# Optimization experiments

Hardware: AMD Instinct MI355X
Metric: run time of the kernel (lower is better)

The kernel has to match this reference:

```python
import jax, jax.numpy as jnp
import numpy as np

B, IN_DIM, UNITS = 16384, 3072, 3072  # batch, input_dim=3*unit1, units=3*unit2


def setup_inputs() -> dict:
    key = jax.random.key(0)
    k1, k2, k3 = jax.random.split(key, 3)
    inputs = jax.random.normal(k1, (B, IN_DIM), dtype=jnp.float32)
    # original init: uniform [0, 0.01) for w, zeros for b (gpe_bias = [0, 0])
    w = jax.random.uniform(k2, (IN_DIM, UNITS), dtype=jnp.float32, minval=0.0, maxval=0.01)
    b = jnp.zeros((UNITS,), dtype=jnp.float32)
    # per-unit binary diagonal mask, stored as [units, input_dim]
    mask = jax.random.randint(k3, (UNITS, IN_DIM), 0, 2, dtype=jnp.int32)
    return {"inputs": inputs, "w": w, "b": b, "mask": mask}


def reference(inputs, w, b, mask):
    # Original: p = transpose(s @ inputs^T, [2,0,1]) -> [batch, units, input_dim]
    #           f = diag_part(p @ w) + b            -> [batch, units]
    # Since s[u] = diag(mask[u]), this is exactly:
    #   f[b,u] = sum_i inputs[b,i] * mask[u,i] * w[i,u] + b[u]
    # i.e. a single masked GEMM with effective weight w * mask^T.
    w_eff = w * mask.T.astype(w.dtype)  # [input_dim, units]
    return inputs @ w_eff + b
```

## Files before the change

### kernel.cpp

```cpp
#include <hip/hip_runtime.h>

#define BATCH 16384
#define KDIM  3072
#define NDIM  3072

typedef __bf16 bf16;
typedef bf16  bf16x8  __attribute__((ext_vector_type(8)));
typedef float f32x16  __attribute__((ext_vector_type(16)));

__device__ __forceinline__ void g2l16(const bf16* g, bf16* l) {
    __builtin_amdgcn_global_load_lds(
        (__attribute__((address_space(1))) unsigned int*)g,
        (__attribute__((address_space(3))) unsigned int*)l,
        16, 0, 0);
}

__global__ __launch_bounds__(256) void cvt_a_kernel(const float* __restrict__ in,
                                                    bf16* __restrict__ out) {
    const long idx = (long)blockIdx.x * 256 + threadIdx.x;
    const float4* in4 = (const float4*)in;
    float4 a = in4[idx * 2];
    float4 b = in4[idx * 2 + 1];
    bf16x8 o;
    o[0] = (bf16)a.x; o[1] = (bf16)a.y; o[2] = (bf16)a.z; o[3] = (bf16)a.w;
    o[4] = (bf16)b.x; o[5] = (bf16)b.y; o[6] = (bf16)b.z; o[7] = (bf16)b.w;
    ((bf16x8*)out)[idx] = o;
}

__global__ __launch_bounds__(256) void weff_kernel(const float* __restrict__ w,
                                                   const int* __restrict__ mask,
                                                   bf16* __restrict__ wt) {
    __shared__ float tile[32][33];
    const int i0 = blockIdx.x * 32;
    const int u0 = blockIdx.y * 32;
    const int tx = threadIdx.x, ty = threadIdx.y;
#pragma unroll
    for (int r = 0; r < 4; r++)
        tile[ty + 8 * r][tx] = w[(long)(i0 + ty + 8 * r) * NDIM + u0 + tx];
    __syncthreads();
#pragma unroll
    for (int r = 0; r < 4; r++) {
        int u = u0 + ty + 8 * r;
        int i = i0 + tx;
        float v = tile[tx][ty + 8 * r] * (float)mask[(long)u * KDIM + i];
        wt[(long)u * KDIM + i] = (bf16)v;
    }
}


#define STAGE_UNIT(Q, KT, KS) do {                                              \
    const long ko_ = (long)(KT) * 64 + ((KS) >> 1) * 32;                        \
    const bf16* gs_ = (((KS) & 1) == 0) ? gA : gB;                              \
    bf16* ds_ = &lds[(Q) * 32768 + ((((KS) & 1) == 0) ? 0 : 16384)              \
                     + ((KS) >> 1) * 8192 + tid * 8];                           \
    g2l16(gs_ + ko_, ds_);                                                      \
    g2l16(gs_ + ko_ + (long)128 * KDIM, ds_ + 4096);                            \
} while (0)

#define PHASE(KS, P, DOSTAGE, KT, VM) do {                                      \
    asm volatile("" ::: "memory");       \
    const bf16* bp_ = &lds[(P) * 32768];                                        \
    const int cOff_ = ((KS) >> 1) * 8192 + (((((KS) & 1) * 2) + kb) ^ sx3) * 8; \
    bf16x8 a0_ = *(const bf16x8*)(bp_ + aOff0 + cOff_);                         \
    bf16x8 a1_ = *(const bf16x8*)(bp_ + aOff1 + cOff_);                         \
    bf16x8 a2_ = *(const bf16x8*)(bp_ + aOff2 + cOff_);                         \
    bf16x8 a3_ = *(const bf16x8*)(bp_ + aOff3 + cOff_);                         \
    bf16x8 b0_ = *(const bf16x8*)(bp_ + bOff0 + cOff_);                         \
    bf16x8 b1_ = *(const bf16x8*)(bp_ + bOff1 + cOff_);                         \
    if (DOSTAGE) { STAGE_UNIT((P) ^ 1, KT, KS); }                               \
    asm volatile("" ::: "memory");          \
    __builtin_amdgcn_s_barrier();                                               \
    asm volatile("s_waitcnt lgkmcnt(0)" ::: "memory");                          \
    __builtin_amdgcn_sched_barrier(0);   \
    __builtin_amdgcn_s_setprio(1);                                              \
    acc[0][0] = __builtin_amdgcn_mfma_f32_32x32x16_bf16(a0_, b0_, acc[0][0], 0, 0, 0); \
    acc[0][1] = __builtin_amdgcn_mfma_f32_32x32x16_bf16(a0_, b1_, acc[0][1], 0, 0, 0); \
    acc[1][0] = __builtin_amdgcn_mfma_f32_32x32x16_bf16(a1_, b0_, acc[1][0], 0, 0, 0); \
    acc[1][1] = __builtin_amdgcn_mfma_f32_32x32x16_bf16(a1_, b1_, acc[1][1], 0, 0, 0); \
    acc[2][0] = __builtin_amdgcn_mfma_f32_32x32x16_bf16(a2_, b0_, acc[2][0], 0, 0, 0); \
    acc[2][1] = __builtin_amdgcn_mfma_f32_32x32x16_bf16(a2_, b1_, acc[2][1], 0, 0, 0); \
    acc[3][0] = __builtin_amdgcn_mfma_f32_32x32x16_bf16(a3_, b0_, acc[3][0], 0, 0, 0); \
    acc[3][1] = __builtin_amdgcn_mfma_f32_32x32x16_bf16(a3_, b1_, acc[3][1], 0, 0, 0); \
    __builtin_amdgcn_s_setprio(0);                                              \
    if ((VM) >= 0)                                                              \
        asm volatile("s_waitcnt vmcnt(%0)" :: "n"((VM) < 0 ? 0 : (VM)) : "memory"); \
    __builtin_amdgcn_s_barrier();                                               \
} while (0)

__global__ __launch_bounds__(512, 2) void gemm_kernel(const bf16* __restrict__ A,
                                                      const bf16* __restrict__ Bt,
                                                      const float* __restrict__ bias,
                                                      float* __restrict__ C) {
    __shared__ __align__(16) bf16 lds[2 * 32768];

    const int tid  = threadIdx.x;
    const int lane = tid & 63;
    const int wv   = tid >> 6;
    const int rl   = lane & 31;
    const int kb   = lane >> 5;
    const int sx3  = rl & 3;

    const int lid = blockIdx.y * gridDim.x + blockIdx.x;
    const int sid = (lid & 7) * 96 + (lid >> 3);
    const long m0 = (long)(sid / 12) * 256;
    const long n0 = (long)(sid % 12) * 256;

    const int waveM = (wv >> 2) * 128;
    const int waveN = (wv & 3) * 64;

    const int srow = tid >> 2;
    const int sc   = (tid & 3) ^ (srow & 3);
    const bf16* gA = A  + (m0 + srow) * KDIM + sc * 8;
    const bf16* gB = Bt + (n0 + srow) * KDIM + sc * 8;

    const int aOff0 = (waveM + 0 * 32 + rl) * 32;
    const int aOff1 = (waveM + 1 * 32 + rl) * 32;
    const int aOff2 = (waveM + 2 * 32 + rl) * 32;
    const int aOff3 = (waveM + 3 * 32 + rl) * 32;
    const int bOff0 = 16384 + (waveN + 0 * 32 + rl) * 32;
    const int bOff1 = 16384 + (waveN + 1 * 32 + rl) * 32;

    f32x16 acc[4][2] = {};

    STAGE_UNIT(0, 0, 0);
    STAGE_UNIT(0, 0, 1);
    STAGE_UNIT(0, 0, 2);
    STAGE_UNIT(0, 0, 3);
    asm volatile("s_waitcnt vmcnt(4)" ::: "memory");
    __builtin_amdgcn_s_barrier();

    const int NT = KDIM / 64;
#pragma unroll 2
    for (int t = 0; t < NT - 1; ++t) {
        const int p = t & 1;
        PHASE(0, p, 1, t + 1, -1);
        PHASE(1, p, 1, t + 1, 4);
        PHASE(2, p, 1, t + 1, -1);
        PHASE(3, p, 1, t + 1, 4);
    }
    PHASE(0, 1, 0, 0, -1);
    PHASE(1, 1, 0, 0, 0);
    PHASE(2, 1, 0, 0, -1);
    PHASE(3, 1, 0, 0, -1);

#pragma unroll
    for (int ni = 0; ni < 2; ++ni) {
        const long col = n0 + waveN + ni * 32 + rl;
        const float bv = bias[col];
#pragma unroll
        for (int mi = 0; mi < 4; ++mi) {
            const long rbase = m0 + waveM + mi * 32 + 4 * kb;
#pragma unroll
            for (int g = 0; g < 4; ++g)
#pragma unroll
                for (int t = 0; t < 4; ++t)
                    C[(rbase + 8 * g + t) * NDIM + col] = acc[mi][ni][4 * g + t] + bv;
        }
    }
}

__global__ __launch_bounds__(256) void naive_kernel(const float* __restrict__ x,
                                                    const float* __restrict__ w,
                                                    const float* __restrict__ bias,
                                                    const int* __restrict__ mask,
                                                    float* __restrict__ out) {
    const long idx = (long)blockIdx.x * 256 + threadIdx.x;
    const long bi = idx / NDIM;
    const int u = (int)(idx % NDIM);
    float s = 0.f;
    for (int k = 0; k < KDIM; k++)
        s += x[bi * KDIM + k] * w[(long)k * NDIM + u] * (float)mask[(long)u * KDIM + k];
    out[idx] = s + bias[u];
}

extern "C" void kernel_launch(void* const* d_in, const int* in_sizes, int n_in,
                              void* d_out, int out_size, void* d_ws, size_t ws_size,
                              hipStream_t stream) {
    const float* x    = (const float*)d_in[0];
    const float* w    = (const float*)d_in[1];
    const float* bias = (const float*)d_in[2];
    const int*   mask = (const int*)d_in[3];
    float* out = (float*)d_out;

    const size_t needA = (size_t)BATCH * KDIM * sizeof(bf16);
    const size_t needW = (size_t)NDIM * KDIM * sizeof(bf16);

    if (ws_size < needA + needW) {
        const long total = (long)BATCH * NDIM;
        naive_kernel<<<(int)(total / 256), 256, 0, stream>>>(x, w, bias, mask, out);
        return;
    }

    bf16* Abf = (bf16*)d_ws;
    bf16* Wt  = (bf16*)((char*)d_ws + needA);

    cvt_a_kernel<<<(BATCH * (KDIM / 8)) / 256, 256, 0, stream>>>(x, Abf);
    weff_kernel<<<dim3(KDIM / 32, NDIM / 32), dim3(32, 8), 0, stream>>>(w, mask, Wt);
    gemm_kernel<<<dim3(NDIM / 256, BATCH / 256), 512, 0, stream>>>(Abf, Wt, bias, out);
}
```

Before: 684.4 us.

## Restructure GEMM main loop with 16x16x32 MFMA, quadrant phases and register fragment reuse

The bf16 GEMM main loop now uses 16x16x32 MFMA instead of 32x32x16. Each wave's output is split into four quadrants computed in separate phases, with A and B fragments held in registers and reused across phases. LDS staging is reorganised into half-tile units with an 8-way XOR swizzle over 64-wide K rows, and loads for later K tiles are interleaved across the phases. The aim is fewer LDS reads per MFMA and better overlap of global-to-LDS transfers with compute, at the cost of more register pressure and a wrap-around prefetch at the loop tail.

```diff
diff --git a/kernel.cpp b/kernel.cpp
--- a/kernel.cpp
+++ b/kernel.cpp
@@ -6,7 +6,7 @@
 
 typedef __bf16 bf16;
 typedef bf16  bf16x8  __attribute__((ext_vector_type(8)));
-typedef float f32x16  __attribute__((ext_vector_type(16)));
+typedef float f32x4   __attribute__((ext_vector_type(4)));
 
 __device__ __forceinline__ void g2l16(const bf16* g, bf16* l) {
     __builtin_amdgcn_global_load_lds(
@@ -47,46 +47,6 @@
     }
 }
 
-
-#define STAGE_UNIT(Q, KT, KS) do {                                              \
-    const long ko_ = (long)(KT) * 64 + ((KS) >> 1) * 32;                        \
-    const bf16* gs_ = (((KS) & 1) == 0) ? gA : gB;                              \
-    bf16* ds_ = &lds[(Q) * 32768 + ((((KS) & 1) == 0) ? 0 : 16384)              \
-                     + ((KS) >> 1) * 8192 + tid * 8];                           \
-    g2l16(gs_ + ko_, ds_);                                                      \
-    g2l16(gs_ + ko_ + (long)128 * KDIM, ds_ + 4096);                            \
-} while (0)
-
-#define PHASE(KS, P, DOSTAGE, KT, VM) do {                                      \
-    asm volatile("" ::: "memory");       \
-    const bf16* bp_ = &lds[(P) * 32768];                                        \
-    const int cOff_ = ((KS) >> 1) * 8192 + (((((KS) & 1) * 2) + kb) ^ sx3) * 8; \
-    bf16x8 a0_ = *(const bf16x8*)(bp_ + aOff0 + cOff_);                         \
-    bf16x8 a1_ = *(const bf16x8*)(bp_ + aOff1 + cOff_);                         \
-    bf16x8 a2_ = *(const bf16x8*)(bp_ + aOff2 + cOff_);                         \
-    bf16x8 a3_ = *(const bf16x8*)(bp_ + aOff3 + cOff_);                         \
-    bf16x8 b0_ = *(const bf16x8*)(bp_ + bOff0 + cOff_);                         \
-    bf16x8 b1_ = *(const bf16x8*)(bp_ + bOff1 + cOff_);                         \
-    if (DOSTAGE) { STAGE_UNIT((P) ^ 1, KT, KS); }                               \
-    asm volatile("" ::: "memory");          \
-    __builtin_amdgcn_s_barrier();                                               \
-    asm volatile("s_waitcnt lgkmcnt(0)" ::: "memory");                          \
-    __builtin_amdgcn_sched_barrier(0);   \
-    __builtin_amdgcn_s_setprio(1);                                              \
-    acc[0][0] = __builtin_amdgcn_mfma_f32_32x32x16_bf16(a0_, b0_, acc[0][0], 0, 0, 0); \
-    acc[0][1] = __builtin_amdgcn_mfma_f32_32x32x16_bf16(a0_, b1_, acc[0][1], 0, 0, 0); \
-    acc[1][0] = __builtin_amdgcn_mfma_f32_32x32x16_bf16(a1_, b0_, acc[1][0], 0, 0, 0); \
-    acc[1][1] = __builtin_amdgcn_mfma_f32_32x32x16_bf16(a1_, b1_, acc[1][1], 0, 0, 0); \
-    acc[2][0] = __builtin_amdgcn_mfma_f32_32x32x16_bf16(a2_, b0_, acc[2][0], 0, 0, 0); \
-    acc[2][1] = __builtin_amdgcn_mfma_f32_32x32x16_bf16(a2_, b1_, acc[2][1], 0, 0, 0); \
-    acc[3][0] = __builtin_amdgcn_mfma_f32_32x32x16_bf16(a3_, b0_, acc[3][0], 0, 0, 0); \
-    acc[3][1] = __builtin_amdgcn_mfma_f32_32x32x16_bf16(a3_, b1_, acc[3][1], 0, 0, 0); \
-    __builtin_amdgcn_s_setprio(0);                                              \
-    if ((VM) >= 0)                                                              \
-        asm volatile("s_waitcnt vmcnt(%0)" :: "n"((VM) < 0 ? 0 : (VM)) : "memory"); \
-    __builtin_amdgcn_s_barrier();                                               \
-} while (0)
-
 __global__ __launch_bounds__(512, 2) void gemm_kernel(const bf16* __restrict__ A,
                                                       const bf16* __restrict__ Bt,
                                                       const float* __restrict__ bias,
@@ -96,67 +56,135 @@
     const int tid  = threadIdx.x;
     const int lane = tid & 63;
     const int wv   = tid >> 6;
-    const int rl   = lane & 31;
-    const int kb   = lane >> 5;
-    const int sx3  = rl & 3;
+    const int l15  = lane & 15;
+    const int l4   = lane >> 4;
+    const int sx   = l15 & 7;
+    const int wm   = (wv >> 2) * 64;
+    const int wn   = (wv & 3) * 32;
 
     const int lid = blockIdx.y * gridDim.x + blockIdx.x;
     const int sid = (lid & 7) * 96 + (lid >> 3);
     const long m0 = (long)(sid / 12) * 256;
     const long n0 = (long)(sid % 12) * 256;
 
-    const int waveM = (wv >> 2) * 128;
-    const int waveN = (wv & 3) * 64;
-
-    const int srow = tid >> 2;
-    const int sc   = (tid & 3) ^ (srow & 3);
-    const bf16* gA = A  + (m0 + srow) * KDIM + sc * 8;
-    const bf16* gB = Bt + (n0 + srow) * KDIM + sc * 8;
-
-    const int aOff0 = (waveM + 0 * 32 + rl) * 32;
-    const int aOff1 = (waveM + 1 * 32 + rl) * 32;
-    const int aOff2 = (waveM + 2 * 32 + rl) * 32;
-    const int aOff3 = (waveM + 3 * 32 + rl) * 32;
-    const int bOff0 = 16384 + (waveN + 0 * 32 + rl) * 32;
-    const int bOff1 = 16384 + (waveN + 1 * 32 + rl) * 32;
-
-    f32x16 acc[4][2] = {};
-
-    STAGE_UNIT(0, 0, 0);
-    STAGE_UNIT(0, 0, 1);
-    STAGE_UNIT(0, 0, 2);
-    STAGE_UNIT(0, 0, 3);
+    const int srow = tid >> 3;
+    const int gsc  = (tid & 7) ^ (srow & 7);
+    const bf16* gAb = A  + (m0 + srow) * (long)KDIM + gsc * 8;
+    const bf16* gBb = Bt + (n0 + srow) * (long)KDIM + gsc * 8;
+
+#define STAGE_A(Q, KT, H) do {                                                  \
+    const bf16* g_ = gAb + (long)((H) * 128) * KDIM + (long)(KT) * 64;          \
+    bf16* d_ = &lds[(Q) * 32768 + (H) * 8192 + tid * 8];                        \
+    g2l16(g_, d_);                                                              \
+    g2l16(g_ + (long)64 * KDIM, d_ + 4096);                                     \
+} while (0)
+#define STAGE_B(Q, KT, H) do {                                                  \
+    const bf16* g_ = gBb + (long)((H) * 128) * KDIM + (long)(KT) * 64;          \
+    bf16* d_ = &lds[(Q) * 32768 + 16384 + (H) * 8192 + tid * 8];                \
+    g2l16(g_, d_);                                                              \
+    g2l16(g_ + (long)64 * KDIM, d_ + 4096);                                     \
+} while (0)
+
+    const int aRow = (wm + l15) * 64;
+    const int bRow = (wn + l15) * 64;
+    const int cc0  = (l4 ^ sx) * 8;
+    const int cc1  = cc0 ^ 32;
+
+    bf16x8 aF[4][2];
+    bf16x8 bF[4][2];
+    f32x4  acc[8][4] = {};
+
+#define RDA(BP, MH)                                                             \
+    _Pragma("unroll") for (int f_ = 0; f_ < 4; ++f_) {                          \
+        aF[f_][0] = *(const bf16x8*)((BP) + (MH) * 8192 + aRow + f_ * 1024 + cc0); \
+        aF[f_][1] = *(const bf16x8*)((BP) + (MH) * 8192 + aRow + f_ * 1024 + cc1); \
+    }
+#define RDB(BP, NH)                                                             \
+    _Pragma("unroll") for (int n_ = 0; n_ < 2; ++n_) {                          \
+        bF[(NH) * 2 + n_][0] = *(const bf16x8*)((BP) + 16384 + (NH) * 8192 + bRow + n_ * 1024 + cc0); \
+        bF[(NH) * 2 + n_][1] = *(const bf16x8*)((BP) + 16384 + (NH) * 8192 + bRow + n_ * 1024 + cc1); \
+    }
+#define MMQ(MH, NH)                                                             \
+    _Pragma("unroll") for (int ks_ = 0; ks_ < 2; ++ks_)                         \
+    _Pragma("unroll") for (int f_ = 0; f_ < 4; ++f_)                            \
+    _Pragma("unroll") for (int n_ = 0; n_ < 2; ++n_)                            \
+        acc[(MH) * 4 + f_][(NH) * 2 + n_] = __builtin_amdgcn_mfma_f32_16x16x32_bf16( \
+            aF[f_][ks_], bF[(NH) * 2 + n_][ks_], acc[(MH) * 4 + f_][(NH) * 2 + n_], 0, 0, 0)
+
+#define PHASE(P, MH, NH, READS, STAGE_STMT, DOVM) do {                          \
+    asm volatile("" ::: "memory");                                              \
+    const bf16* bp_ = &lds[(P) * 32768];                                        \
+    READS;                                                                      \
+    STAGE_STMT;                                                                 \
+    asm volatile("" ::: "memory");                                              \
+    __builtin_amdgcn_s_barrier();                                               \
+    asm volatile("s_waitcnt lgkmcnt(0)" ::: "memory");                          \
+    __builtin_amdgcn_sched_barrier(0);                                          \
+    __builtin_amdgcn_s_setprio(1);                                              \
+    MMQ(MH, NH);                                                                \
+    __builtin_amdgcn_s_setprio(0);                                              \
+    if (DOVM) asm volatile("s_waitcnt vmcnt(4)" ::: "memory");                  \
+    __builtin_amdgcn_s_barrier();                                               \
+} while (0)
+
+#define RD_AB(MH, NH) RDA(bp_, MH); RDB(bp_, NH)
+#define RD_ONLYB(NH)  RDB(bp_, NH)
+#define RD_ONLYA(MH)  RDA(bp_, MH)
+#define RD_NONE       ((void)0)
+
+    STAGE_A(0, 0, 0);
+    STAGE_B(0, 0, 0);
+    STAGE_B(0, 0, 1);
+    STAGE_A(0, 0, 1);
+    STAGE_A(1, 1, 0);
+    STAGE_B(1, 1, 0);
     asm volatile("s_waitcnt vmcnt(4)" ::: "memory");
     __builtin_amdgcn_s_barrier();
 
     const int NT = KDIM / 64;
-#pragma unroll 2
-    for (int t = 0; t < NT - 1; ++t) {
-        const int p = t & 1;
-        PHASE(0, p, 1, t + 1, -1);
-        PHASE(1, p, 1, t + 1, 4);
-        PHASE(2, p, 1, t + 1, -1);
-        PHASE(3, p, 1, t + 1, 4);
-    }
-    PHASE(0, 1, 0, 0, -1);
-    PHASE(1, 1, 0, 0, 0);
-    PHASE(2, 1, 0, 0, -1);
-    PHASE(3, 1, 0, 0, -1);
-
-#pragma unroll
-    for (int ni = 0; ni < 2; ++ni) {
-        const long col = n0 + waveN + ni * 32 + rl;
-        const float bv = bias[col];
-#pragma unroll
-        for (int mi = 0; mi < 4; ++mi) {
-            const long rbase = m0 + waveM + mi * 32 + 4 * kb;
-#pragma unroll
-            for (int g = 0; g < 4; ++g)
-#pragma unroll
-                for (int t = 0; t < 4; ++t)
-                    C[(rbase + 8 * g + t) * NDIM + col] = acc[mi][ni][4 * g + t] + bv;
+#pragma unroll 1
+    for (int t = 0; t < NT; t += 2) {
+        const int k1 = t + 1;
+        const int k2 = (t + 2 < NT) ? t + 2 : 0;
+        const int k3 = (t + 3 < NT) ? t + 3 : t + 3 - NT;
+        PHASE(0, 0, 0, RD_AB(0, 0),  STAGE_B(1, k1, 1), 0);
+        PHASE(0, 0, 1, RD_ONLYB(1),  STAGE_A(1, k1, 1), 0);
+        PHASE(0, 1, 0, RD_ONLYA(1),  STAGE_A(0, k2, 0), 0);
+        PHASE(0, 1, 1, RD_NONE,      STAGE_B(0, k2, 0), 1);
+        PHASE(1, 0, 0, RD_AB(0, 0),  STAGE_B(0, k2, 1), 0);
+        PHASE(1, 0, 1, RD_ONLYB(1),  STAGE_A(0, k2, 1), 0);
+        PHASE(1, 1, 0, RD_ONLYA(1),  STAGE_A(1, k3, 0), 0);
+        PHASE(1, 1, 1, RD_NONE,      STAGE_B(1, k3, 0), 1);
+    }
+    asm volatile("s_waitcnt vmcnt(0)" ::: "memory");
+
+    float bv[4];
+#pragma unroll
+    for (int n_ = 0; n_ < 4; ++n_) {
+        const long gc = n0 + ((n_ < 2) ? (wn + n_ * 16) : (128 + wn + (n_ - 2) * 16)) + l15;
+        bv[n_] = bias[gc];
+    }
+#pragma unroll
+    for (int f_ = 0; f_ < 8; ++f_) {
+        const long gm = m0 + ((f_ < 4) ? (wm + f_ * 16) : (128 + wm + (f_ - 4) * 16)) + l4 * 4;
+#pragma unroll
+        for (int n_ = 0; n_ < 4; ++n_) {
+            const long gc = n0 + ((n_ < 2) ? (wn + n_ * 16) : (128 + wn + (n_ - 2) * 16)) + l15;
+#pragma unroll
+            for (int r_ = 0; r_ < 4; ++r_)
+                C[(gm + r_) * NDIM + gc] = acc[f_][n_][r_] + bv[n_];
         }
     }
+#undef STAGE_A
+#undef STAGE_B
+#undef RDA
+#undef RDB
+#undef MMQ
+#undef PHASE
+#undef RD_AB
+#undef RD_ONLYB
+#undef RD_ONLYA
+#undef RD_NONE
 }
 
 __global__ __launch_bounds__(256) void naive_kernel(const float* __restrict__ x,
```

Result: faster. 610.2 us (-10.8%).
